# Kernel optimization log

Hardware: AMD Instinct MI355X
Metric: run time of the kernel (lower is better)

Reference implementation:

```python
import jax, jax.numpy as jnp
import numpy as np

B, D, OUT, K = 2048, 256, 256, 16


def setup_inputs() -> dict:
    key = jax.random.key(0)
    k1, k2, k3, k4 = jax.random.split(key, 4)
    x = jax.random.normal(k1, (B, D), dtype=jnp.float32)
    values = jax.random.uniform(k2, (OUT, D, K), dtype=jnp.float32, minval=-0.05, maxval=0.05)
    skip_w = jax.random.normal(k3, (OUT, D), dtype=jnp.float32) * (1.0 / np.sqrt(D).astype(np.float32))
    skip_b = jax.random.normal(k4, (OUT,), dtype=jnp.float32) * 0.01
    return {"x": x, "values": values, "skip_w": skip_w, "skip_b": skip_b}


def reference(x, values, skip_w, skip_b):
    # x: (B, D); values: (OUT, D, K); skip_w: (OUT, D); skip_b: (OUT,)
    num_knots = values.shape[-1]
    grid = jnp.linspace(-1.0, 1.0, num_knots)  # (K,)
    xc = jnp.clip(x, -1.0, 1.0)
    # torch.bucketize(x, grid) with right=False == searchsorted side='left'
    right = jnp.searchsorted(grid, xc, side='left')
    left = jnp.clip(right - 1, 0, num_knots - 2)  # (B, D)
    right = left + 1
    g0 = grid[left]
    g1 = grid[right]
    w = (xc - g0) / (g1 - g0 + 1e-12)  # (B, D)
    # Gather spline values per (sample, input-dim) knot bucket.
    vt = jnp.transpose(values, (1, 2, 0))  # (D, K, OUT)
    dim_idx = jnp.arange(xc.shape[1])[None, :]  # (1, D)
    v_left = vt[dim_idx, left]    # (B, D, OUT)
    v_right = vt[dim_idx, right]  # (B, D, OUT)
    # Linear interpolation + sum over input dims.
    y = jnp.sum((1.0 - w)[..., None] * v_left + w[..., None] * v_right, axis=1)  # (B, OUT)
    # Skip connection on the clamped input (torch reassigns x = clamp(x) first).
    return y + xc @ skip_w.T + skip_b
```

## Files before the change

kernel.cpp:

```cpp
#include <hip/hip_runtime.h>
#include <hip/hip_bf16.h>


namespace {
constexpr int Bsz  = 2048;
constexpr int Din  = 256;
constexpr int Dout = 256;
constexpr int Kn   = 16;
constexpr int KKNOT = Din * Kn;
constexpr int KB    = KKNOT / 32;
constexpr float INV_H = 7.5f;
constexpr float Hgrid = 2.0f / 15.0f;

constexpr int NSTEP = KKNOT / 64;
constexpr int SXS   = 260;
}

typedef __attribute__((ext_vector_type(8))) short shortx8;
typedef __attribute__((ext_vector_type(4))) float floatx4;

__device__ __forceinline__ unsigned int f2bf(float f) {
  __hip_bfloat16 h = __float2bfloat16(f);
  return (unsigned int)*reinterpret_cast<unsigned short*>(&h);
}
__device__ __forceinline__ float clamp1(float v) {
  return fminf(1.f, fmaxf(-1.f, v));
}
__device__ __forceinline__ unsigned int packbf(unsigned int e0, unsigned int e1) {
  return (e1 & 0xffff0000u) | (e0 >> 16);
}
__device__ __forceinline__ unsigned int rnd(float f) {
  return __float_as_uint(f) + 0x8000u;
}

__device__ __forceinline__ void buildA(unsigned short* dst, float xv, float h0) {
  const float t = (clamp1(xv) + 1.f) * INV_H;
  unsigned int e[8];
  #pragma unroll
  for (int h = 0; h < 8; ++h)
    e[h] = rnd(fmaxf(0.f, 1.f - fabsf(t - (h0 + (float)h))));
  *(uint4*)dst = make_uint4(packbf(e[0], e[1]), packbf(e[2], e[3]),
                            packbf(e[4], e[5]), packbf(e[6], e[7]));
}

__device__ __forceinline__ void mstep(const unsigned short* aBuf,
                                      const uint4 b0, const uint4 b1,
                                      const int o00, const int o01,
                                      const int o10, const int o11,
                                      floatx4& acc0, floatx4& acc1) {
  const shortx8 a00 = *(const shortx8*)(aBuf + o00);
  const shortx8 a10 = *(const shortx8*)(aBuf + o10);
  const shortx8 a01 = *(const shortx8*)(aBuf + o01);
  const shortx8 a11 = *(const shortx8*)(aBuf + o11);
  union { uint4 u; shortx8 s; } c0, c1;
  c0.u = b0; c1.u = b1;
  acc0 = __builtin_amdgcn_mfma_f32_16x16x32_bf16(a00, c0.s, acc0, 0, 0, 0);
  acc1 = __builtin_amdgcn_mfma_f32_16x16x32_bf16(a10, c0.s, acc1, 0, 0, 0);
  acc0 = __builtin_amdgcn_mfma_f32_16x16x32_bf16(a01, c1.s, acc0, 0, 0, 0);
  acc1 = __builtin_amdgcn_mfma_f32_16x16x32_bf16(a11, c1.s, acc1, 0, 0, 0);
}

__global__ __launch_bounds__(256) void kan_prep(
    const float* __restrict__ values, const float* __restrict__ skip_w,
    unsigned short* __restrict__ Wf) {
  const int tid = blockIdx.x * 256 + threadIdx.x;
  const int q  = tid & 3;
  const int n  = (tid >> 2) & 15;
  const int og = (tid >> 6) & 15;
  const int kb = tid >> 10;
  const int o  = og * 16 + n;
  const int k0 = kb * 32 + q * 8;
  const int d  = k0 >> 4;
  const float h0 = (float)(k0 & 15);
  const float sw = skip_w[o * Din + d];
  const float* src = values + (size_t)o * KKNOT + k0;
  const float4 v0 = *(const float4*)src;
  const float4 v1 = *(const float4*)(src + 4);
  float e[8] = {v0.x, v0.y, v0.z, v0.w, v1.x, v1.y, v1.z, v1.w};
  #pragma unroll
  for (int j = 0; j < 8; ++j)
    e[j] = fmaf(-1.f + (h0 + (float)j) * Hgrid, sw, e[j]);
  const size_t chunk = (size_t)kb * 1024 + og * 64 + q * 16 + n;
  *(uint4*)(Wf + chunk * 8) = make_uint4(
      f2bf(e[0]) | (f2bf(e[1]) << 16), f2bf(e[2]) | (f2bf(e[3]) << 16),
      f2bf(e[4]) | (f2bf(e[5]) << 16), f2bf(e[6]) | (f2bf(e[7]) << 16));
}

__global__ __launch_bounds__(256) void kan_gemm_full(
    const float* __restrict__ x, const unsigned short* __restrict__ Wf,
    const float* __restrict__ skip_b, float* __restrict__ out) {
  __shared__ float sx[32 * SXS];
  __shared__ __align__(16) unsigned short aLds[2][32 * 64];

  const int tid  = threadIdx.x;
  const int wave = tid >> 6, lane = tid & 63;
  const int mi   = blockIdx.x & 63;
  const int oq   = blockIdx.x >> 6;
  const int m0   = mi * 32;
  const int og   = oq * 4 + wave;
  const int lrow = lane & 15, lq = lane >> 4;

  const int brow = tid >> 3;
  const int bseg = tid & 7;
  const int kbi  = bseg >> 2;
  const int dsel = (bseg >> 1) & 1;
  const float h0 = (float)((bseg & 1) * 8);

  const int swz   = lrow & 7;
  const int o00   = lrow * 64 + ((lq ^ swz) << 3);
  const int o01   = lrow * 64 + (((4 | lq) ^ swz) << 3);
  const int o10   = o00 + 16 * 64;
  const int o11   = o01 + 16 * 64;
  const int awoff = brow * 64 + ((bseg ^ (brow & 7)) << 3);

  const uint4* B = (const uint4*)Wf;

  floatx4 acc0 = {}, acc1 = {};
  uint4 bb0[2], bb1[2];

  for (int i = tid; i < 32 * 64; i += 256) {
    const int r = i >> 6, c = i & 63;
    *(float4*)&sx[r * SXS + c * 4] = *(const float4*)(x + (size_t)(m0 + r) * Din + c * 4);
  }
  bb0[0] = B[(size_t)0 * 1024 + og * 64 + lane];
  bb0[1] = B[(size_t)1 * 1024 + og * 64 + lane];
  bb1[0] = B[(size_t)2 * 1024 + og * 64 + lane];
  bb1[1] = B[(size_t)3 * 1024 + og * 64 + lane];
  __syncthreads();

  buildA(&aLds[0][awoff], sx[brow * SXS + 2 * kbi + dsel], h0);

  for (int s = 0; s < NSTEP; s += 2) {
    {
      const uint4 c0 = bb0[0], c1 = bb0[1];
      if (s + 2 < NSTEP) {
        bb0[0] = B[(size_t)(2 * (s + 2)    ) * 1024 + og * 64 + lane];
        bb0[1] = B[(size_t)(2 * (s + 2) + 1) * 1024 + og * 64 + lane];
      }
      __syncthreads();
      buildA(&aLds[1][awoff], sx[brow * SXS + 4 * (s + 1) + 2 * kbi + dsel], h0);
      mstep(aLds[0], c0, c1, o00, o01, o10, o11, acc0, acc1);
    }
    {
      const uint4 c0 = bb1[0], c1 = bb1[1];
      if (s + 3 < NSTEP) {
        bb1[0] = B[(size_t)(2 * (s + 3)    ) * 1024 + og * 64 + lane];
        bb1[1] = B[(size_t)(2 * (s + 3) + 1) * 1024 + og * 64 + lane];
      }
      __syncthreads();
      if (s + 2 < NSTEP)
        buildA(&aLds[0][awoff], sx[brow * SXS + 4 * (s + 2) + 2 * kbi + dsel], h0);
      mstep(aLds[1], c0, c1, o00, o01, o10, o11, acc0, acc1);
    }
  }

  const int ocol = og * 16 + lrow;
  const int r0   = m0 + lq * 4;
  const float sb = skip_b[ocol];
  #pragma unroll
  for (int j = 0; j < 4; ++j)
    out[(size_t)(r0 + j) * Dout + ocol] = acc0[j] + sb;
  #pragma unroll
  for (int j = 0; j < 4; ++j)
    out[(size_t)(r0 + 16 + j) * Dout + ocol] = acc1[j] + sb;
}

__device__ __forceinline__ void knot_interp(float xraw, float& xv, float& w, int& l) {
  xv = fminf(1.0f, fmaxf(-1.0f, xraw));
  float t = (xv + 1.0f) * INV_H;
  l = (int)ceilf(t) - 1;
  l = l < 0 ? 0 : (l > Kn - 2 ? Kn - 2 : l);
  float g0 = -1.0f + Hgrid * (float)l;
  w = (xv - g0) * INV_H;
}

__global__ __launch_bounds__(256) void prep_transpose(
    const float* __restrict__ values, const float* __restrict__ skip_w,
    float* __restrict__ vt, float* __restrict__ swt) {
  int idx = blockIdx.x * blockDim.x + threadIdx.x;
  if (idx < Din * Kn * Dout) {
    int k = idx & (Kn - 1);
    int d = (idx >> 4) & (Din - 1);
    int o = idx >> 12;
    vt[(d * Kn + k) * Dout + o] = values[idx];
  }
  if (idx < Dout * Din) {
    int d = idx & (Din - 1);
    int o = idx >> 8;
    swt[d * Dout + o] = skip_w[idx];
  }
}

__global__ __launch_bounds__(256) void kan_main(
    const float* __restrict__ x, const float* __restrict__ vt,
    const float* __restrict__ swt, const float* __restrict__ skip_b,
    float* __restrict__ out) {
  __shared__ float s_w[4][Din];
  __shared__ float s_x[4][Din];
  __shared__ int   s_l[4][Din];
  const int tid = threadIdx.x;
  const int b0  = blockIdx.x * 4;
  for (int i = tid; i < 4 * Din; i += 256) {
    int bb = i >> 8;
    int d  = i & (Din - 1);
    float xv, w; int l;
    knot_interp(x[(b0 + bb) * Din + d], xv, w, l);
    s_w[bb][d] = w; s_x[bb][d] = xv; s_l[bb][d] = l;
  }
  __syncthreads();
  const int g = tid >> 6, lane = tid & 63;
  const int o = lane << 2, b = b0 + g;
  float4 acc = make_float4(0.f, 0.f, 0.f, 0.f);
  for (int d = 0; d < Din; ++d) {
    const float w = s_w[g][d], xv = s_x[g][d];
    const int l = s_l[g][d];
    const float* base = vt + (d * Kn + l) * Dout + o;
    const float4 vl = *(const float4*)(base);
    const float4 vr = *(const float4*)(base + Dout);
    const float4 sw = *(const float4*)(swt + d * Dout + o);
    acc.x = fmaf(xv, sw.x, fmaf(w, vr.x - vl.x, acc.x + vl.x));
    acc.y = fmaf(xv, sw.y, fmaf(w, vr.y - vl.y, acc.y + vl.y));
    acc.z = fmaf(xv, sw.z, fmaf(w, vr.z - vl.z, acc.z + vl.z));
    acc.w = fmaf(xv, sw.w, fmaf(w, vr.w - vl.w, acc.w + vl.w));
  }
  const float4 bias = *(const float4*)(skip_b + o);
  acc.x += bias.x; acc.y += bias.y; acc.z += bias.z; acc.w += bias.w;
  *(float4*)(out + (size_t)b * Dout + o) = acc;
}

extern "C" void kernel_launch(void* const* d_in, const int* in_sizes, int n_in,
                              void* d_out, int out_size, void* d_ws, size_t ws_size,
                              hipStream_t stream) {
  (void)in_sizes; (void)n_in; (void)out_size;
  const float* x      = (const float*)d_in[0];
  const float* values = (const float*)d_in[1];
  const float* skip_w = (const float*)d_in[2];
  const float* skip_b = (const float*)d_in[3];
  float* out = (float*)d_out;

  const size_t wf_bytes = (size_t)Dout * KKNOT * sizeof(unsigned short);
  const size_t need_fb  = (size_t)(Din * Kn * Dout + Din * Dout) * sizeof(float);

  if (ws_size >= wf_bytes) {
    unsigned short* Wf = (unsigned short*)d_ws;
    kan_prep<<<(KB * 1024) / 256, 256, 0, stream>>>(values, skip_w, Wf);
    kan_gemm_full<<<256, 256, 0, stream>>>(x, Wf, skip_b, out);
  } else if (ws_size >= need_fb) {
    float* vt  = (float*)d_ws;
    float* swt = vt + Din * Kn * Dout;
    prep_transpose<<<(Din * Kn * Dout + 255) / 256, 256, 0, stream>>>(values, skip_w, vt, swt);
    kan_main<<<Bsz / 4, 256, 0, stream>>>(x, vt, swt, skip_b, out);
  }
}
```

Before: 88.69 us.

## Materialize bf16 hat-basis A matrix in prep kernel, stream both operands from global

The prep kernel now also expands x into a full bf16 hat-function matrix (B x D*K) in MFMA fragment order in workspace. The GEMM kernel then drops LDS staging and barriers and loads both A and B fragments straight from global with a four-deep register prefetch, using 512 blocks with a 2x2 wave tiling. This removes per-block A construction and syncthreads from the GEMM. In exchange it writes and rereads a 16 MB A matrix through memory, and needs a larger workspace.

```diff
diff --git a/kernel.cpp b/kernel.cpp
--- a/kernel.cpp
+++ b/kernel.cpp
@@ -11,9 +11,6 @@
 constexpr int KB    = KKNOT / 32;
 constexpr float INV_H = 7.5f;
 constexpr float Hgrid = 2.0f / 15.0f;
-
-constexpr int NSTEP = KKNOT / 64;
-constexpr int SXS   = 260;
 }
 
 typedef __attribute__((ext_vector_type(8))) short shortx8;
@@ -33,136 +30,113 @@
   return __float_as_uint(f) + 0x8000u;
 }
 
-__device__ __forceinline__ void buildA(unsigned short* dst, float xv, float h0) {
+__device__ __forceinline__ uint4 hat8(float xv, float h0) {
   const float t = (clamp1(xv) + 1.f) * INV_H;
   unsigned int e[8];
   #pragma unroll
   for (int h = 0; h < 8; ++h)
     e[h] = rnd(fmaxf(0.f, 1.f - fabsf(t - (h0 + (float)h))));
-  *(uint4*)dst = make_uint4(packbf(e[0], e[1]), packbf(e[2], e[3]),
-                            packbf(e[4], e[5]), packbf(e[6], e[7]));
-}
-
-__device__ __forceinline__ void mstep(const unsigned short* aBuf,
-                                      const uint4 b0, const uint4 b1,
-                                      const int o00, const int o01,
-                                      const int o10, const int o11,
-                                      floatx4& acc0, floatx4& acc1) {
-  const shortx8 a00 = *(const shortx8*)(aBuf + o00);
-  const shortx8 a10 = *(const shortx8*)(aBuf + o10);
-  const shortx8 a01 = *(const shortx8*)(aBuf + o01);
-  const shortx8 a11 = *(const shortx8*)(aBuf + o11);
-  union { uint4 u; shortx8 s; } c0, c1;
-  c0.u = b0; c1.u = b1;
-  acc0 = __builtin_amdgcn_mfma_f32_16x16x32_bf16(a00, c0.s, acc0, 0, 0, 0);
-  acc1 = __builtin_amdgcn_mfma_f32_16x16x32_bf16(a10, c0.s, acc1, 0, 0, 0);
-  acc0 = __builtin_amdgcn_mfma_f32_16x16x32_bf16(a01, c1.s, acc0, 0, 0, 0);
-  acc1 = __builtin_amdgcn_mfma_f32_16x16x32_bf16(a11, c1.s, acc1, 0, 0, 0);
-}
-
-__global__ __launch_bounds__(256) void kan_prep(
-    const float* __restrict__ values, const float* __restrict__ skip_w,
-    unsigned short* __restrict__ Wf) {
+  return make_uint4(packbf(e[0], e[1]), packbf(e[2], e[3]),
+                    packbf(e[4], e[5]), packbf(e[6], e[7]));
+}
+
+__global__ __launch_bounds__(256) void kan_prep2(
+    const float* __restrict__ x, const float* __restrict__ values,
+    const float* __restrict__ skip_w, unsigned short* __restrict__ Wf,
+    unsigned short* __restrict__ Af) {
   const int tid = blockIdx.x * 256 + threadIdx.x;
-  const int q  = tid & 3;
-  const int n  = (tid >> 2) & 15;
-  const int og = (tid >> 6) & 15;
-  const int kb = tid >> 10;
-  const int o  = og * 16 + n;
-  const int k0 = kb * 32 + q * 8;
-  const int d  = k0 >> 4;
-  const float h0 = (float)(k0 & 15);
-  const float sw = skip_w[o * Din + d];
-  const float* src = values + (size_t)o * KKNOT + k0;
-  const float4 v0 = *(const float4*)src;
-  const float4 v1 = *(const float4*)(src + 4);
-  float e[8] = {v0.x, v0.y, v0.z, v0.w, v1.x, v1.y, v1.z, v1.w};
-  #pragma unroll
-  for (int j = 0; j < 8; ++j)
-    e[j] = fmaf(-1.f + (h0 + (float)j) * Hgrid, sw, e[j]);
-  const size_t chunk = (size_t)kb * 1024 + og * 64 + q * 16 + n;
-  *(uint4*)(Wf + chunk * 8) = make_uint4(
-      f2bf(e[0]) | (f2bf(e[1]) << 16), f2bf(e[2]) | (f2bf(e[3]) << 16),
-      f2bf(e[4]) | (f2bf(e[5]) << 16), f2bf(e[6]) | (f2bf(e[7]) << 16));
-}
-
-__global__ __launch_bounds__(256) void kan_gemm_full(
-    const float* __restrict__ x, const unsigned short* __restrict__ Wf,
+  {
+    const int q  = tid & 3;
+    const int n  = (tid >> 2) & 15;
+    const int og = (tid >> 6) & 15;
+    const int kb = tid >> 10;
+    const int o  = og * 16 + n;
+    const int k0 = kb * 32 + q * 8;
+    const int d  = k0 >> 4;
+    const float h0 = (float)(k0 & 15);
+    const float sw = skip_w[o * Din + d];
+    const float* src = values + (size_t)o * KKNOT + k0;
+    const float4 v0 = *(const float4*)src;
+    const float4 v1 = *(const float4*)(src + 4);
+    float e[8] = {v0.x, v0.y, v0.z, v0.w, v1.x, v1.y, v1.z, v1.w};
+    #pragma unroll
+    for (int j = 0; j < 8; ++j)
+      e[j] = fmaf(-1.f + (h0 + (float)j) * Hgrid, sw, e[j]);
+    const size_t chunk = (size_t)kb * 1024 + og * 64 + q * 16 + n;
+    *(uint4*)(Wf + chunk * 8) = make_uint4(
+        f2bf(e[0]) | (f2bf(e[1]) << 16), f2bf(e[2]) | (f2bf(e[3]) << 16),
+        f2bf(e[4]) | (f2bf(e[5]) << 16), f2bf(e[6]) | (f2bf(e[7]) << 16));
+  }
+  {
+    const int lane  = threadIdx.x & 63;
+    const int wslot = blockIdx.x * 4 + (threadIdx.x >> 6);
+    const int lrow  = lane & 15, lq = lane >> 4;
+    uint4* A4 = (uint4*)Af;
+    #pragma unroll
+    for (int ci = 0; ci < 8; ++ci) {
+      const int chunk = wslot * 8 + ci;
+      const int kb = chunk >> 7;
+      const int rp = chunk & 127;
+      const int row = rp * 16 + lrow;
+      const int d   = kb * 2 + (lq >> 1);
+      const float h0 = (float)((lq & 1) * 8);
+      const float xv = x[(size_t)row * Din + d];
+      A4[(size_t)chunk * 64 + lane] = hat8(xv, h0);
+    }
+  }
+}
+
+__global__ __launch_bounds__(256) void kan_gemm2(
+    const unsigned short* __restrict__ Af, const unsigned short* __restrict__ Wf,
     const float* __restrict__ skip_b, float* __restrict__ out) {
-  __shared__ float sx[32 * SXS];
-  __shared__ __align__(16) unsigned short aLds[2][32 * 64];
-
   const int tid  = threadIdx.x;
   const int wave = tid >> 6, lane = tid & 63;
   const int mi   = blockIdx.x & 63;
-  const int oq   = blockIdx.x >> 6;
-  const int m0   = mi * 32;
-  const int og   = oq * 4 + wave;
-  const int lrow = lane & 15, lq = lane >> 4;
-
-  const int brow = tid >> 3;
-  const int bseg = tid & 7;
-  const int kbi  = bseg >> 2;
-  const int dsel = (bseg >> 1) & 1;
-  const float h0 = (float)((bseg & 1) * 8);
-
-  const int swz   = lrow & 7;
-  const int o00   = lrow * 64 + ((lq ^ swz) << 3);
-  const int o01   = lrow * 64 + (((4 | lq) ^ swz) << 3);
-  const int o10   = o00 + 16 * 64;
-  const int o11   = o01 + 16 * 64;
-  const int awoff = brow * 64 + ((bseg ^ (brow & 7)) << 3);
-
-  const uint4* B = (const uint4*)Wf;
-
-  floatx4 acc0 = {}, acc1 = {};
-  uint4 bb0[2], bb1[2];
-
-  for (int i = tid; i < 32 * 64; i += 256) {
-    const int r = i >> 6, c = i & 63;
-    *(float4*)&sx[r * SXS + c * 4] = *(const float4*)(x + (size_t)(m0 + r) * Din + c * 4);
-  }
-  bb0[0] = B[(size_t)0 * 1024 + og * 64 + lane];
-  bb0[1] = B[(size_t)1 * 1024 + og * 64 + lane];
-  bb1[0] = B[(size_t)2 * 1024 + og * 64 + lane];
-  bb1[1] = B[(size_t)3 * 1024 + og * 64 + lane];
-  __syncthreads();
-
-  buildA(&aLds[0][awoff], sx[brow * SXS + 2 * kbi + dsel], h0);
-
-  for (int s = 0; s < NSTEP; s += 2) {
-    {
-      const uint4 c0 = bb0[0], c1 = bb0[1];
-      if (s + 2 < NSTEP) {
-        bb0[0] = B[(size_t)(2 * (s + 2)    ) * 1024 + og * 64 + lane];
-        bb0[1] = B[(size_t)(2 * (s + 2) + 1) * 1024 + og * 64 + lane];
-      }
-      __syncthreads();
-      buildA(&aLds[1][awoff], sx[brow * SXS + 4 * (s + 1) + 2 * kbi + dsel], h0);
-      mstep(aLds[0], c0, c1, o00, o01, o10, o11, acc0, acc1);
-    }
-    {
-      const uint4 c0 = bb1[0], c1 = bb1[1];
-      if (s + 3 < NSTEP) {
-        bb1[0] = B[(size_t)(2 * (s + 3)    ) * 1024 + og * 64 + lane];
-        bb1[1] = B[(size_t)(2 * (s + 3) + 1) * 1024 + og * 64 + lane];
-      }
-      __syncthreads();
-      if (s + 2 < NSTEP)
-        buildA(&aLds[0][awoff], sx[brow * SXS + 4 * (s + 2) + 2 * kbi + dsel], h0);
-      mstep(aLds[1], c0, c1, o00, o01, o10, o11, acc0, acc1);
-    }
-  }
-
-  const int ocol = og * 16 + lrow;
-  const int r0   = m0 + lq * 4;
-  const float sb = skip_b[ocol];
+  const int nj   = blockIdx.x >> 6;
+  const int wr   = wave >> 1, wc = wave & 1;
+  const int rp   = mi * 2 + wr;
+  const int cp   = nj * 2 + wc;
+
+  const uint4* A4 = (const uint4*)Af;
+  const uint4* B4 = (const uint4*)Wf;
+  const size_t aoff = (size_t)rp * 64 + lane;
+  const size_t boff = (size_t)cp * 64 + lane;
+
+  union U { uint4 u; shortx8 s; };
+  floatx4 accE = {}, accO = {};
+  uint4 a0, a1, a2, a3, b0, b1, b2, b3;
+
+  a0 = A4[(size_t)0 * 8192 + aoff]; b0 = B4[(size_t)0 * 1024 + boff];
+  a1 = A4[(size_t)1 * 8192 + aoff]; b1 = B4[(size_t)1 * 1024 + boff];
+  a2 = A4[(size_t)2 * 8192 + aoff]; b2 = B4[(size_t)2 * 1024 + boff];
+  a3 = A4[(size_t)3 * 8192 + aoff]; b3 = B4[(size_t)3 * 1024 + boff];
+
+  for (int kb = 0; kb < KB; kb += 4) {
+    U au, bu;
+    au.u = a0; bu.u = b0;
+    accE = __builtin_amdgcn_mfma_f32_16x16x32_bf16(au.s, bu.s, accE, 0, 0, 0);
+    if (kb + 4 < KB) { a0 = A4[(size_t)(kb + 4) * 8192 + aoff];
+                       b0 = B4[(size_t)(kb + 4) * 1024 + boff]; }
+    au.u = a1; bu.u = b1;
+    accO = __builtin_amdgcn_mfma_f32_16x16x32_bf16(au.s, bu.s, accO, 0, 0, 0);
+    if (kb + 5 < KB) { a1 = A4[(size_t)(kb + 5) * 8192 + aoff];
+                       b1 = B4[(size_t)(kb + 5) * 1024 + boff]; }
+    au.u = a2; bu.u = b2;
+    accE = __builtin_amdgcn_mfma_f32_16x16x32_bf16(au.s, bu.s, accE, 0, 0, 0);
+    if (kb + 6 < KB) { a2 = A4[(size_t)(kb + 6) * 8192 + aoff];
+                       b2 = B4[(size_t)(kb + 6) * 1024 + boff]; }
+    au.u = a3; bu.u = b3;
+    accO = __builtin_amdgcn_mfma_f32_16x16x32_bf16(au.s, bu.s, accO, 0, 0, 0);
+    if (kb + 7 < KB) { a3 = A4[(size_t)(kb + 7) * 8192 + aoff];
+                       b3 = B4[(size_t)(kb + 7) * 1024 + boff]; }
+  }
+
+  const int col  = cp * 16 + (lane & 15);
+  const int row0 = mi * 32 + wr * 16 + (lane >> 4) * 4;
+  const float sb = skip_b[col];
   #pragma unroll
   for (int j = 0; j < 4; ++j)
-    out[(size_t)(r0 + j) * Dout + ocol] = acc0[j] + sb;
-  #pragma unroll
-  for (int j = 0; j < 4; ++j)
-    out[(size_t)(r0 + 16 + j) * Dout + ocol] = acc1[j] + sb;
+    out[(size_t)(row0 + j) * Dout + col] = (accE[j] + accO[j]) + sb;
 }
 
 __device__ __forceinline__ void knot_interp(float xraw, float& xv, float& w, int& l) {
@@ -239,12 +213,15 @@
   float* out = (float*)d_out;
 
   const size_t wf_bytes = (size_t)Dout * KKNOT * sizeof(unsigned short);
+  const size_t af_bytes = (size_t)Bsz * KKNOT * sizeof(unsigned short);
+  const size_t need2    = wf_bytes + af_bytes;
   const size_t need_fb  = (size_t)(Din * Kn * Dout + Din * Dout) * sizeof(float);
 
-  if (ws_size >= wf_bytes) {
+  if (ws_size >= need2) {
     unsigned short* Wf = (unsigned short*)d_ws;
-    kan_prep<<<(KB * 1024) / 256, 256, 0, stream>>>(values, skip_w, Wf);
-    kan_gemm_full<<<256, 256, 0, stream>>>(x, Wf, skip_b, out);
+    unsigned short* Af = (unsigned short*)((char*)d_ws + wf_bytes);
+    kan_prep2<<<512, 256, 0, stream>>>(x, values, skip_w, Wf, Af);
+    kan_gemm2<<<512, 256, 0, stream>>>(Af, Wf, skip_b, out);
   } else if (ws_size >= need_fb) {
     float* vt  = (float*)d_ws;
     float* swt = vt + Din * Kn * Dout;
```

Result: faster. 86.75 us (-2.2%).
